# Optimization experiments

Measured on AMD Instinct MI355X. Metric: run time of the kernel, lower is better.

The kernel has to match this reference:

```python
import jax, jax.numpy as jnp
import numpy as np

B, L1, L2, D = 64, 512, 512, 256
NEG_INF = -1e10


def _leaky(x):
    return jax.nn.leaky_relu(x, negative_slope=0.01)


def setup_inputs() -> dict:
    key = jax.random.key(0)
    ks = jax.random.split(key, 12)
    s = 1.0 / np.sqrt(D)
    s2 = 1.0 / np.sqrt(2 * D)
    return {
        "r1": jax.random.normal(ks[0], (B, L1, D), jnp.float32),
        "r2": jax.random.normal(ks[1], (B, L2, D), jnp.float32),
        "mask1": jax.random.randint(ks[2], (B, L1, 1), 0, 2, jnp.int32),
        "mask2": jax.random.randint(ks[3], (B, L2, 1), 0, 2, jnp.int32),
        # mlp params (shared for r1 and r2, as in the torch module)
        "W1": jax.random.uniform(ks[4], (D, D), jnp.float32, -s, s),
        "b1": jnp.zeros((D,), jnp.float32),
        "W2": jax.random.uniform(ks[5], (D, D), jnp.float32, -s, s),
        "b2": jnp.zeros((D,), jnp.float32),
        # compare params
        "Wc1": jax.random.uniform(ks[6], (2 * D, D), jnp.float32, -s2, s2),
        "bc1": jnp.zeros((D,), jnp.float32),
        "Wc2": jax.random.uniform(ks[7], (D, D), jnp.float32, -s, s),
        "bc2": jnp.zeros((D,), jnp.float32),
    }


def _mlp(x, W1, b1, W2, b2):
    return _leaky(_leaky(x @ W1 + b1) @ W2 + b2)


def _compare(x, Wc1, bc1, Wc2, bc2):
    return _leaky(_leaky(x @ Wc1 + bc1) @ Wc2 + bc2)


def reference(r1, r2, mask1, mask2, W1, b1, W2, b2, Wc1, bc1, Wc2, bc2):
    # dropout layers are identity in eval mode
    m1 = mask1.astype(jnp.float32)  # [B,L1,1]
    m2 = mask2.astype(jnp.float32)  # [B,L2,1]

    h1 = _mlp(r1, W1, b1, W2, b2) * m1  # [B,L1,D]
    h2 = _mlp(r2, W1, b1, W2, b2) * m2  # [B,L2,D]

    lens1 = m1.sum(axis=1)  # [B,1]
    lens2 = m2.sum(axis=1)  # [B,1]

    # pairwise validity: matmul of expanded masks is D * outer(m1, m2);
    # only the sign is used downstream.
    pair = m1[:, :, 0][:, :, None] * m2[:, :, 0][:, None, :]  # [B,L1,L2]
    valid = pair > 0
    mask_inf = jnp.where(valid, 0.0, NEG_INF)

    o = jnp.einsum('bld,bmd->blm', h1, h2) + mask_inf  # [B,L1,L2]
    vf = valid.astype(o.dtype)
    o1 = jax.nn.softmax(o, axis=2) * vf
    o2 = jax.nn.softmax(o, axis=1) * vf

    r1_c = jnp.einsum('blm,bmd->bld', o1, h2)  # [B,L1,D]
    r2_c = jnp.einsum('blm,bld->bmd', o2, h1)  # [B,L2,D]

    r1_cmp = _compare(jnp.concatenate([h1, r1_c], axis=-1), Wc1, bc1, Wc2, bc2)
    r2_cmp = _compare(jnp.concatenate([h2, r2_c], axis=-1), Wc1, bc1, Wc2, bc2)

    r1_pool = (r1_cmp * m1).sum(axis=1) / lens1  # [B,D]
    r2_pool = (r2_cmp * m2).sum(axis=1) / lens2  # [B,D]
    return (r1_pool, r2_pool)
```

## Files before the change

### kernel.cpp

```cpp
#include <hip/hip_runtime.h>
#include <math.h>


using frag  = __attribute__((ext_vector_type(8))) short;
using f32x4 = __attribute__((ext_vector_type(4))) float;

constexpr int  LDK = 40;
constexpr int  KS  = 32;
constexpr long E   = 16777216L;

__device__ __forceinline__ float leaky(float x){ return x > 0.f ? x : 0.01f * x; }

__device__ __forceinline__ unsigned bf16_rne(float f){
    unsigned x = __float_as_uint(f);
    return (x + 0x7fffu + ((x >> 16) & 1u)) >> 16;
}
__device__ __forceinline__ unsigned pack_pair(float v){
    unsigned hi = bf16_rne(v);
    float fhi = __uint_as_float(hi << 16);
    unsigned lo = bf16_rne(v - fhi);
    return (hi << 16) | lo;
}

template<int AMODE, int BMODE, int EPI, int DUALA>
__global__ __launch_bounds__(512, 4)
void gemm_k(const unsigned* __restrict__ pa, const unsigned* __restrict__ pa2,
            const unsigned* __restrict__ pb, const float* __restrict__ bias,
            unsigned* __restrict__ pc,
            const int* __restrict__ mk1, const int* __restrict__ mk2,
            int M, int N, int K, int K1,
            int lda, int ldb, int ldc,
            long sA, long sB, long sC)
{
    __shared__ short As_hi[128 * LDK], As_lo[128 * LDK];
    __shared__ short Bs_hi[128 * LDK], Bs_lo[128 * LDK];

    const int z = blockIdx.z;
    const long aoff = (long)z * sA, boff = (long)z * sB, coff = (long)z * sC;
    const int m0 = blockIdx.x * 128, n0 = blockIdx.y * 128;
    const int tid  = threadIdx.x;
    const int lane = tid & 63;
    const int w    = tid >> 6;
    const int wr = w >> 2, wc = w & 3;
    const int lrow = lane & 15, lk = (lane >> 4) * 8;

    f32x4 acc[4][2];
#pragma unroll
    for (int i = 0; i < 4; ++i)
#pragma unroll
        for (int j = 0; j < 2; ++j) acc[i][j] = (f32x4){0.f, 0.f, 0.f, 0.f};

    for (int k0 = 0; k0 < K; k0 += KS) {
        if (AMODE == 0) {
            const int row = tid >> 2, k8 = (tid & 3) * 8;
            const unsigned* base = pa + aoff;
            int kk = k0;
            if (DUALA) { if (k0 >= K1) { base = pa2; kk = k0 - K1; } }
            const unsigned* src = base + (long)(m0 + row) * lda + kk + k8;
            uint4 wa = *(const uint4*)src;
            uint4 wb = *(const uint4*)(src + 4);
            uint4 hs, ls;
            hs.x = __builtin_amdgcn_perm(wa.y, wa.x, 0x07060302u);
            ls.x = __builtin_amdgcn_perm(wa.y, wa.x, 0x05040100u);
            hs.y = __builtin_amdgcn_perm(wa.w, wa.z, 0x07060302u);
            ls.y = __builtin_amdgcn_perm(wa.w, wa.z, 0x05040100u);
            hs.z = __builtin_amdgcn_perm(wb.y, wb.x, 0x07060302u);
            ls.z = __builtin_amdgcn_perm(wb.y, wb.x, 0x05040100u);
            hs.w = __builtin_amdgcn_perm(wb.w, wb.z, 0x07060302u);
            ls.w = __builtin_amdgcn_perm(wb.w, wb.z, 0x05040100u);
            *(uint4*)&As_hi[row * LDK + k8] = hs;
            *(uint4*)&As_lo[row * LDK + k8] = ls;
        } else if (AMODE == 1) {
            const int row = tid >> 2, k8 = (tid & 3) * 8;
            const int gr = m0 + row;
            const float* fb_ = (gr < 32768) ? ((const float*)pa  + (long)gr * lda)
                                            : ((const float*)pa2 + (long)(gr - 32768) * lda);
            const float* src = fb_ + k0 + k8;
            float4 fa = *(const float4*)src, fbv = *(const float4*)(src + 4);
            float f[8] = {fa.x, fa.y, fa.z, fa.w, fbv.x, fbv.y, fbv.z, fbv.w};
            unsigned hi[8], lo[8];
#pragma unroll
            for (int j = 0; j < 8; ++j) {
                hi[j] = bf16_rne(f[j]);
                lo[j] = bf16_rne(f[j] - __uint_as_float(hi[j] << 16));
            }
            uint4 hs = {hi[0] | (hi[1] << 16), hi[2] | (hi[3] << 16), hi[4] | (hi[5] << 16), hi[6] | (hi[7] << 16)};
            uint4 ls = {lo[0] | (lo[1] << 16), lo[2] | (lo[3] << 16), lo[4] | (lo[5] << 16), lo[6] | (lo[7] << 16)};
            *(uint4*)&As_hi[row * LDK + k8] = hs;
            *(uint4*)&As_lo[row * LDK + k8] = ls;
        } else {
            if (tid < 256) {
                const int k2 = ((tid >> 4) & 15) * 2, m8 = (tid & 15) * 8;
                const unsigned* s0 = pa + aoff + (long)(k0 + k2) * lda + m0 + m8;
                const unsigned* s1 = s0 + lda;
                uint4 a0 = *(const uint4*)s0, a1 = *(const uint4*)(s0 + 4);
                uint4 b0 = *(const uint4*)s1, b1 = *(const uint4*)(s1 + 4);
                unsigned wk[8]  = {a0.x, a0.y, a0.z, a0.w, a1.x, a1.y, a1.z, a1.w};
                unsigned wk1[8] = {b0.x, b0.y, b0.z, b0.w, b1.x, b1.y, b1.z, b1.w};
#pragma unroll
                for (int i = 0; i < 8; ++i) {
                    unsigned hw = __builtin_amdgcn_perm(wk1[i], wk[i], 0x07060302u);
                    unsigned lw = __builtin_amdgcn_perm(wk1[i], wk[i], 0x05040100u);
                    *(unsigned*)&As_hi[(m8 + i) * LDK + k2] = hw;
                    *(unsigned*)&As_lo[(m8 + i) * LDK + k2] = lw;
                }
            }
        }
        if (BMODE == 1) {
            const int row = tid >> 2, k8 = (tid & 3) * 8;
            const unsigned* src = pb + boff + (long)(n0 + row) * ldb + k0 + k8;
            uint4 wa = *(const uint4*)src;
            uint4 wb = *(const uint4*)(src + 4);
            uint4 hs, ls;
            hs.x = __builtin_amdgcn_perm(wa.y, wa.x, 0x07060302u);
            ls.x = __builtin_amdgcn_perm(wa.y, wa.x, 0x05040100u);
            hs.y = __builtin_amdgcn_perm(wa.w, wa.z, 0x07060302u);
            ls.y = __builtin_amdgcn_perm(wa.w, wa.z, 0x05040100u);
            hs.z = __builtin_amdgcn_perm(wb.y, wb.x, 0x07060302u);
            ls.z = __builtin_amdgcn_perm(wb.y, wb.x, 0x05040100u);
            hs.w = __builtin_amdgcn_perm(wb.w, wb.z, 0x07060302u);
            ls.w = __builtin_amdgcn_perm(wb.w, wb.z, 0x05040100u);
            *(uint4*)&Bs_hi[row * LDK + k8] = hs;
            *(uint4*)&Bs_lo[row * LDK + k8] = ls;
        } else if (BMODE == 0) {
            if (tid < 256) {
                const int k2 = ((tid >> 4) & 15) * 2, n8 = (tid & 15) * 8;
                const float* s0 = (const float*)pb + boff + (long)(k0 + k2) * ldb + n0 + n8;
                const float* s1 = s0 + ldb;
                float4 a0 = *(const float4*)s0, a1 = *(const float4*)(s0 + 4);
                float4 b0 = *(const float4*)s1, b1 = *(const float4*)(s1 + 4);
                float f0[8] = {a0.x, a0.y, a0.z, a0.w, a1.x, a1.y, a1.z, a1.w};
                float f1[8] = {b0.x, b0.y, b0.z, b0.w, b1.x, b1.y, b1.z, b1.w};
#pragma unroll
                for (int i = 0; i < 8; ++i) {
                    unsigned h0 = bf16_rne(f0[i]);
                    unsigned l0 = bf16_rne(f0[i] - __uint_as_float(h0 << 16));
                    unsigned h1 = bf16_rne(f1[i]);
                    unsigned l1 = bf16_rne(f1[i] - __uint_as_float(h1 << 16));
                    *(unsigned*)&Bs_hi[(n8 + i) * LDK + k2] = h0 | (h1 << 16);
                    *(unsigned*)&Bs_lo[(n8 + i) * LDK + k2] = l0 | (l1 << 16);
                }
            }
        } else {
            if (tid < 256) {
                const int k2 = ((tid >> 4) & 15) * 2, n8 = (tid & 15) * 8;
                const unsigned* s0 = pb + boff + (long)(k0 + k2) * ldb + n0 + n8;
                const unsigned* s1 = s0 + ldb;
                uint4 a0 = *(const uint4*)s0, a1 = *(const uint4*)(s0 + 4);
                uint4 b0 = *(const uint4*)s1, b1 = *(const uint4*)(s1 + 4);
                unsigned wk[8]  = {a0.x, a0.y, a0.z, a0.w, a1.x, a1.y, a1.z, a1.w};
                unsigned wk1[8] = {b0.x, b0.y, b0.z, b0.w, b1.x, b1.y, b1.z, b1.w};
#pragma unroll
                for (int i = 0; i < 8; ++i) {
                    unsigned hw = __builtin_amdgcn_perm(wk1[i], wk[i], 0x07060302u);
                    unsigned lw = __builtin_amdgcn_perm(wk1[i], wk[i], 0x05040100u);
                    *(unsigned*)&Bs_hi[(n8 + i) * LDK + k2] = hw;
                    *(unsigned*)&Bs_lo[(n8 + i) * LDK + k2] = lw;
                }
            }
        }
        __syncthreads();

        frag ah[4], al[4], bh[2], bl[2];
#pragma unroll
        for (int mi = 0; mi < 4; ++mi) {
            const int r = (wr * 64 + mi * 16 + lrow) * LDK + lk;
            ah[mi] = *(const frag*)&As_hi[r];
            al[mi] = *(const frag*)&As_lo[r];
        }
#pragma unroll
        for (int ni = 0; ni < 2; ++ni) {
            const int r = (wc * 32 + ni * 16 + lrow) * LDK + lk;
            bh[ni] = *(const frag*)&Bs_hi[r];
            bl[ni] = *(const frag*)&Bs_lo[r];
        }
#pragma unroll
        for (int mi = 0; mi < 4; ++mi)
#pragma unroll
            for (int ni = 0; ni < 2; ++ni) {
                acc[mi][ni] = __builtin_amdgcn_mfma_f32_16x16x32_bf16(ah[mi], bh[ni], acc[mi][ni], 0, 0, 0);
                acc[mi][ni] = __builtin_amdgcn_mfma_f32_16x16x32_bf16(ah[mi], bl[ni], acc[mi][ni], 0, 0, 0);
                acc[mi][ni] = __builtin_amdgcn_mfma_f32_16x16x32_bf16(al[mi], bh[ni], acc[mi][ni], 0, 0, 0);
            }
        __syncthreads();
    }

    float bvv[2];
    if (EPI == 2 || EPI == 3 || EPI == 4) {
#pragma unroll
        for (int ni = 0; ni < 2; ++ni) bvv[ni] = bias[n0 + wc * 32 + ni * 16 + lrow];
    }
#pragma unroll
    for (int mi = 0; mi < 4; ++mi)
#pragma unroll
        for (int ni = 0; ni < 2; ++ni) {
            const int col = n0 + wc * 32 + ni * 16 + lrow;
#pragma unroll
            for (int r = 0; r < 4; ++r) {
                const int row = m0 + wr * 64 + mi * 16 + (lane >> 4) * 4 + r;
                float v = acc[mi][ni][r];
                if (EPI == 2 || EPI == 3 || EPI == 4) v = leaky(v + bvv[ni]);
                if (EPI == 3) v *= (float)(row < 32768 ? mk1[row] : mk2[row - 32768]);
                const long off = coff + (long)row * ldc + col;
                if (EPI == 0 || EPI == 4) ((float*)pc)[off] = v;
                else                      pc[off] = pack_pair(v);
            }
        }
}

__global__ __launch_bounds__(256)
void softmax_row_k(const unsigned* __restrict__ S, const int* __restrict__ m1,
                   const int* __restrict__ m2, unsigned* __restrict__ O)
{
    const int tid = threadIdx.x;
    const int wid = tid >> 6, lane = tid & 63;
    const int gr = blockIdx.x * 4 + wid;
    const int b = gr >> 9, l = gr & 511;
    const unsigned* srow = S + (long)gr * 512;
    unsigned* orow = O + (long)gr * 512;
    const int rowvalid = m1[(long)b * 512 + l];
    const int* m2b = m2 + (long)b * 512;
    const int c8 = lane * 8;
    int4 ma = *(const int4*)(m2b + c8);
    int4 mb_ = *(const int4*)(m2b + c8 + 4);
    uint4 va = *(const uint4*)(srow + c8);
    uint4 vb = *(const uint4*)(srow + c8 + 4);
    float v[8] = {__uint_as_float(va.x), __uint_as_float(va.y), __uint_as_float(va.z), __uint_as_float(va.w),
                  __uint_as_float(vb.x), __uint_as_float(vb.y), __uint_as_float(vb.z), __uint_as_float(vb.w)};
    int mk[8] = {ma.x, ma.y, ma.z, ma.w, mb_.x, mb_.y, mb_.z, mb_.w};
    float mx = -3e38f;
#pragma unroll
    for (int j = 0; j < 8; ++j) if (mk[j]) mx = fmaxf(mx, v[j]);
#pragma unroll
    for (int o = 32; o; o >>= 1) mx = fmaxf(mx, __shfl_xor(mx, o));
    if (!rowvalid || mx < -1e30f) {
        uint4 zz = {0u, 0u, 0u, 0u};
        *(uint4*)(orow + c8) = zz; *(uint4*)(orow + c8 + 4) = zz;
        return;
    }
    float e[8]; float s = 0.f;
#pragma unroll
    for (int j = 0; j < 8; ++j) { e[j] = mk[j] ? __expf(v[j] - mx) : 0.f; s += e[j]; }
#pragma unroll
    for (int o = 32; o; o >>= 1) s += __shfl_xor(s, o);
    const float inv = 1.f / s;
    uint4 oa, ob;
    oa.x = pack_pair(e[0] * inv); oa.y = pack_pair(e[1] * inv);
    oa.z = pack_pair(e[2] * inv); oa.w = pack_pair(e[3] * inv);
    ob.x = pack_pair(e[4] * inv); ob.y = pack_pair(e[5] * inv);
    ob.z = pack_pair(e[6] * inv); ob.w = pack_pair(e[7] * inv);
    *(uint4*)(orow + c8) = oa;
    *(uint4*)(orow + c8 + 4) = ob;
}

__global__ __launch_bounds__(1024)
void softmax_col_k(const unsigned* __restrict__ S, const int* __restrict__ m1,
                   const int* __restrict__ m2, unsigned* __restrict__ O)
{
    __shared__ float red[16][64];
    __shared__ int m1s[512];
    const int b = blockIdx.y;
    const int c0 = blockIdx.x * 64;
    const int tid = threadIdx.x;
    const int c = tid & 63, rq = tid >> 6;
    if (tid < 512) m1s[tid] = m1[(long)b * 512 + tid];
    const int ac = m2[(long)b * 512 + c0 + c];
    const unsigned* Sb = S + (long)b * 512 * 512 + c0 + c;
    unsigned* Ob = O + (long)b * 512 * 512 + c0 + c;
    __syncthreads();

    float v[32];
#pragma unroll
    for (int g = 0; g < 32; ++g) {
        const int r = g * 16 + rq;
        float val = __uint_as_float(Sb[(long)r * 512]);
        v[g] = m1s[r] ? val : -3e38f;
    }
    float mx = -3e38f;
#pragma unroll
    for (int g = 0; g < 32; ++g) mx = fmaxf(mx, v[g]);
    red[rq][c] = mx;
    __syncthreads();
    float M = -3e38f;
#pragma unroll
    for (int i = 0; i < 16; ++i) M = fmaxf(M, red[i][c]);
    __syncthreads();
    float s = 0.f;
#pragma unroll
    for (int g = 0; g < 32; ++g) {
        float e = (v[g] > -1e30f) ? __expf(v[g] - M) : 0.f;
        v[g] = e;
        s += e;
    }
    red[rq][c] = s;
    __syncthreads();
    s = 0.f;
#pragma unroll
    for (int i = 0; i < 16; ++i) s += red[i][c];
    const float inv = (ac && s > 0.f) ? 1.f / s : 0.f;
#pragma unroll
    for (int g = 0; g < 32; ++g) {
        const int r = g * 16 + rq;
        Ob[(long)r * 512] = pack_pair(v[g] * inv);
    }
}

__global__ __launch_bounds__(256)
void pool_part_k(const float* __restrict__ RC, const int* __restrict__ m1,
                 const int* __restrict__ m2, float* __restrict__ part)
{
    const int rs = blockIdx.x, b = blockIdx.y, seg = blockIdx.z;
    const int* mb = (seg ? m2 : m1) + (long)b * 512;
    const float* base = RC + ((long)seg * 32768 + (long)b * 512) * 256;
    const int n = threadIdx.x;
    float acc = 0.f;
    for (int l = rs * 64; l < rs * 64 + 64; ++l)
        if (mb[l]) acc += base[(long)l * 256 + n];
    part[(((long)seg * 64 + b) * 8 + rs) * 256 + n] = acc;
}

__global__ __launch_bounds__(256)
void pool_red_k(const float* __restrict__ part, const int* __restrict__ m1,
                const int* __restrict__ m2, float* __restrict__ out)
{
    __shared__ float cr[256];
    const int g = blockIdx.x;
    const int seg = g >> 6, b = g & 63;
    const int n = threadIdx.x;
    const int* mb = (seg ? m2 : m1) + (long)b * 512;
    float s = 0.f;
#pragma unroll
    for (int i = 0; i < 8; ++i) s += part[((long)g * 8 + i) * 256 + n];
    float cpart = (float)(mb[n] + mb[n + 256]);
    cr[n] = cpart;
    __syncthreads();
    for (int o = 128; o; o >>= 1) { if (n < o) cr[n] += cr[n + o]; __syncthreads(); }
    out[(long)g * 256 + n] = s / cr[0];
}

extern "C" void kernel_launch(void* const* d_in, const int* in_sizes, int n_in,
                              void* d_out, int out_size, void* d_ws, size_t ws_size,
                              hipStream_t stream)
{
    const float* r1  = (const float*)d_in[0];
    const float* r2  = (const float*)d_in[1];
    const int*   mk1 = (const int*)d_in[2];
    const int*   mk2 = (const int*)d_in[3];
    const float* W1  = (const float*)d_in[4];
    const float* b1  = (const float*)d_in[5];
    const float* W2  = (const float*)d_in[6];
    const float* b2  = (const float*)d_in[7];
    const float* Wc1 = (const float*)d_in[8];
    const float* bc1 = (const float*)d_in[9];
    const float* Wc2 = (const float*)d_in[10];
    const float* bc2 = (const float*)d_in[11];
    float* out = (float*)d_out;

    unsigned* S0 = (unsigned*)d_ws;
    unsigned* S1 = S0 + E;
    unsigned* S2 = S0 + 2 * E;
    unsigned* S3 = S0 + 3 * E;
    const long H2OFF = 32768L * 256;

    dim3 blk(512), sblk(256);

    gemm_k<1,0,2,0><<<dim3(512,2,1), blk, 0, stream>>>(
        (const unsigned*)r1, (const unsigned*)r2, (const unsigned*)W1, b1, S1,
        nullptr, nullptr, 65536,256,256,0, 256,256,256, 0,0,0);
    gemm_k<0,0,3,0><<<dim3(512,2,1), blk, 0, stream>>>(
        S1, nullptr, (const unsigned*)W2, b2, S2,
        mk1, mk2, 65536,256,256,0, 256,256,256, 0,0,0);
    gemm_k<0,1,0,0><<<dim3(4,4,64), blk, 0, stream>>>(
        S2, nullptr, S2 + H2OFF, nullptr, S0,
        nullptr, nullptr, 512,512,256,0, 256,256,512, 131072,131072,262144);
    softmax_col_k<<<dim3(8,64), dim3(1024), 0, stream>>>(S0, mk1, mk2, S1);
    softmax_row_k<<<8192, sblk, 0, stream>>>(S0, mk1, mk2, S0);
    gemm_k<0,2,1,0><<<dim3(4,2,64), blk, 0, stream>>>(
        S0, nullptr, S2 + H2OFF, nullptr, S3,
        nullptr, nullptr, 512,256,512,0, 512,256,256, 262144,131072,131072);
    gemm_k<2,2,1,0><<<dim3(4,2,64), blk, 0, stream>>>(
        S1, nullptr, S2, nullptr, S3 + H2OFF,
        nullptr, nullptr, 512,256,512,0, 512,256,256, 262144,131072,131072);
    gemm_k<0,0,2,1><<<dim3(512,2,1), blk, 0, stream>>>(
        S2, S3, (const unsigned*)Wc1, bc1, S0,
        nullptr, nullptr, 65536,256,512,256, 256,256,256, 0,0,0);
    gemm_k<0,0,4,0><<<dim3(512,2,1), blk, 0, stream>>>(
        S0, nullptr, (const unsigned*)Wc2, bc2, S1,
        nullptr, nullptr, 65536,256,256,0, 256,256,256, 0,0,0);
    pool_part_k<<<dim3(8,64,2), sblk, 0, stream>>>((const float*)S1, mk1, mk2, (float*)S2);
    pool_red_k<<<128, sblk, 0, stream>>>((const float*)S2, mk1, mk2, out);
}
```

Before: 633.3 us.

## Store split-bf16 operands as separate hi/lo planes and load via global_load_lds

Intermediate tensors move from packed hi|lo 32-bit words to two separate bf16 planes, and weights are pre-transposed and split by a small conversion kernel. This lets the GEMM load A/B tiles directly into LDS with global_load_lds in fragment-ordered layout, removing the per-element perm unpacking and the padded LDS layout. The softmax outputs are written as transposed planes, so the column-softmax result feeds the GEMM the same way as the row one. The cost is extra conversion launches, strided 2-byte scalar loads for the transposed B path, and scattered short stores in the epilogues.

```diff
diff --git a/kernel.cpp b/kernel.cpp
--- a/kernel.cpp
+++ b/kernel.cpp
@@ -5,9 +5,7 @@
 using frag  = __attribute__((ext_vector_type(8))) short;
 using f32x4 = __attribute__((ext_vector_type(4))) float;
 
-constexpr int  LDK = 40;
-constexpr int  KS  = 32;
-constexpr long E   = 16777216L;
+constexpr long E = 16777216L;
 
 __device__ __forceinline__ float leaky(float x){ return x > 0.f ? x : 0.01f * x; }
 
@@ -15,34 +13,27 @@
     unsigned x = __float_as_uint(f);
     return (x + 0x7fffu + ((x >> 16) & 1u)) >> 16;
 }
-__device__ __forceinline__ unsigned pack_pair(float v){
-    unsigned hi = bf16_rne(v);
-    float fhi = __uint_as_float(hi << 16);
-    unsigned lo = bf16_rne(v - fhi);
-    return (hi << 16) | lo;
+
+__device__ __forceinline__ void gload16(const void* g, void* l){
+    __builtin_amdgcn_global_load_lds((const __attribute__((address_space(1))) void*)g,
+                                     (__attribute__((address_space(3))) void*)l, 16, 0, 0);
 }
 
 template<int AMODE, int BMODE, int EPI, int DUALA>
 __global__ __launch_bounds__(512, 4)
-void gemm_k(const unsigned* __restrict__ pa, const unsigned* __restrict__ pa2,
-            const unsigned* __restrict__ pb, const float* __restrict__ bias,
-            unsigned* __restrict__ pc,
+void gemm_k(const short* __restrict__ pa, const short* __restrict__ pa2,
+            const short* __restrict__ pb, const float* __restrict__ bias,
+            short* __restrict__ pc,
             const int* __restrict__ mk1, const int* __restrict__ mk2,
-            int M, int N, int K, int K1,
-            int lda, int ldb, int ldc,
-            long sA, long sB, long sC)
-{
-    __shared__ short As_hi[128 * LDK], As_lo[128 * LDK];
-    __shared__ short Bs_hi[128 * LDK], Bs_lo[128 * LDK];
-
+            int K, int K1, int lda, int ldb, int ldc,
+            long sA, long sB, long sC, long PSA, long PSB, long PSC)
+{
+    __shared__ __align__(16) short Ah[4096], Al[4096], Bh[4096], Bl[4096];
     const int z = blockIdx.z;
+    const int m0 = blockIdx.x * 128, n0 = blockIdx.y * 128;
+    const int tid = threadIdx.x, lane = tid & 63, w = tid >> 6;
+    const int wr = w >> 2, wc = w & 3;
     const long aoff = (long)z * sA, boff = (long)z * sB, coff = (long)z * sC;
-    const int m0 = blockIdx.x * 128, n0 = blockIdx.y * 128;
-    const int tid  = threadIdx.x;
-    const int lane = tid & 63;
-    const int w    = tid >> 6;
-    const int wr = w >> 2, wc = w & 3;
-    const int lrow = lane & 15, lk = (lane >> 4) * 8;
 
     f32x4 acc[4][2];
 #pragma unroll
@@ -50,137 +41,72 @@
 #pragma unroll
         for (int j = 0; j < 2; ++j) acc[i][j] = (f32x4){0.f, 0.f, 0.f, 0.f};
 
-    for (int k0 = 0; k0 < K; k0 += KS) {
+    for (int k0 = 0; k0 < K; k0 += 32) {
         if (AMODE == 0) {
-            const int row = tid >> 2, k8 = (tid & 3) * 8;
-            const unsigned* base = pa + aoff;
-            int kk = k0;
-            if (DUALA) { if (k0 >= K1) { base = pa2; kk = k0 - K1; } }
-            const unsigned* src = base + (long)(m0 + row) * lda + kk + k8;
-            uint4 wa = *(const uint4*)src;
-            uint4 wb = *(const uint4*)(src + 4);
-            uint4 hs, ls;
-            hs.x = __builtin_amdgcn_perm(wa.y, wa.x, 0x07060302u);
-            ls.x = __builtin_amdgcn_perm(wa.y, wa.x, 0x05040100u);
-            hs.y = __builtin_amdgcn_perm(wa.w, wa.z, 0x07060302u);
-            ls.y = __builtin_amdgcn_perm(wa.w, wa.z, 0x05040100u);
-            hs.z = __builtin_amdgcn_perm(wb.y, wb.x, 0x07060302u);
-            ls.z = __builtin_amdgcn_perm(wb.y, wb.x, 0x05040100u);
-            hs.w = __builtin_amdgcn_perm(wb.w, wb.z, 0x07060302u);
-            ls.w = __builtin_amdgcn_perm(wb.w, wb.z, 0x05040100u);
-            *(uint4*)&As_hi[row * LDK + k8] = hs;
-            *(uint4*)&As_lo[row * LDK + k8] = ls;
-        } else if (AMODE == 1) {
-            const int row = tid >> 2, k8 = (tid & 3) * 8;
-            const int gr = m0 + row;
-            const float* fb_ = (gr < 32768) ? ((const float*)pa  + (long)gr * lda)
-                                            : ((const float*)pa2 + (long)(gr - 32768) * lda);
-            const float* src = fb_ + k0 + k8;
-            float4 fa = *(const float4*)src, fbv = *(const float4*)(src + 4);
-            float f[8] = {fa.x, fa.y, fa.z, fa.w, fbv.x, fbv.y, fbv.z, fbv.w};
-            unsigned hi[8], lo[8];
+            const short* base = pa + aoff; int kk = k0;
+            if (DUALA) { if (k0 >= K1) { base = pa2 + aoff; kk = k0 - K1; } }
+            const short* s = base + (long)(m0 + w * 16 + (lane & 15)) * lda + kk + (lane >> 4) * 8;
+            gload16(s,       &Ah[w * 512]);
+            gload16(s + PSA, &Al[w * 512]);
+        } else {
+            const int gr = m0 + w * 16 + (lane & 15);
+            const float* f = (gr < 32768 ? (const float*)pa + (long)gr * lda
+                                         : (const float*)pa2 + (long)(gr - 32768) * lda)
+                             + k0 + (lane >> 4) * 8;
+            float4 u = *(const float4*)f, v4 = *(const float4*)(f + 4);
+            float fv[8] = {u.x, u.y, u.z, u.w, v4.x, v4.y, v4.z, v4.w};
+            unsigned hu[8], lu[8];
 #pragma unroll
             for (int j = 0; j < 8; ++j) {
-                hi[j] = bf16_rne(f[j]);
-                lo[j] = bf16_rne(f[j] - __uint_as_float(hi[j] << 16));
+                hu[j] = bf16_rne(fv[j]);
+                lu[j] = bf16_rne(fv[j] - __uint_as_float(hu[j] << 16));
             }
-            uint4 hs = {hi[0] | (hi[1] << 16), hi[2] | (hi[3] << 16), hi[4] | (hi[5] << 16), hi[6] | (hi[7] << 16)};
-            uint4 ls = {lo[0] | (lo[1] << 16), lo[2] | (lo[3] << 16), lo[4] | (lo[5] << 16), lo[6] | (lo[7] << 16)};
-            *(uint4*)&As_hi[row * LDK + k8] = hs;
-            *(uint4*)&As_lo[row * LDK + k8] = ls;
+            uint4 hs = {hu[0] | (hu[1] << 16), hu[2] | (hu[3] << 16), hu[4] | (hu[5] << 16), hu[6] | (hu[7] << 16)};
+            uint4 ls = {lu[0] | (lu[1] << 16), lu[2] | (lu[3] << 16), lu[4] | (lu[5] << 16), lu[6] | (lu[7] << 16)};
+            *(uint4*)&Ah[w * 512 + lane * 8] = hs;
+            *(uint4*)&Al[w * 512 + lane * 8] = ls;
+        }
+        if (BMODE == 0) {
+            const short* s = pb + boff + (long)(n0 + w * 16 + (lane & 15)) * ldb + k0 + (lane >> 4) * 8;
+            gload16(s,       &Bh[w * 512]);
+            gload16(s + PSB, &Bl[w * 512]);
         } else {
-            if (tid < 256) {
-                const int k2 = ((tid >> 4) & 15) * 2, m8 = (tid & 15) * 8;
-                const unsigned* s0 = pa + aoff + (long)(k0 + k2) * lda + m0 + m8;
-                const unsigned* s1 = s0 + lda;
-                uint4 a0 = *(const uint4*)s0, a1 = *(const uint4*)(s0 + 4);
-                uint4 b0 = *(const uint4*)s1, b1 = *(const uint4*)(s1 + 4);
-                unsigned wk[8]  = {a0.x, a0.y, a0.z, a0.w, a1.x, a1.y, a1.z, a1.w};
-                unsigned wk1[8] = {b0.x, b0.y, b0.z, b0.w, b1.x, b1.y, b1.z, b1.w};
-#pragma unroll
-                for (int i = 0; i < 8; ++i) {
-                    unsigned hw = __builtin_amdgcn_perm(wk1[i], wk[i], 0x07060302u);
-                    unsigned lw = __builtin_amdgcn_perm(wk1[i], wk[i], 0x05040100u);
-                    *(unsigned*)&As_hi[(m8 + i) * LDK + k2] = hw;
-                    *(unsigned*)&As_lo[(m8 + i) * LDK + k2] = lw;
-                }
+            const int kg = tid >> 7, nn = tid & 127;
+            const short* s = pb + boff + (long)(k0 + kg * 8) * ldb + n0 + nn;
+            unsigned hh[8], ll[8];
+#pragma unroll
+            for (int i = 0; i < 8; ++i) {
+                hh[i] = (unsigned short)s[(long)i * ldb];
+                ll[i] = (unsigned short)s[(long)i * ldb + PSB];
             }
-        }
-        if (BMODE == 1) {
-            const int row = tid >> 2, k8 = (tid & 3) * 8;
-            const unsigned* src = pb + boff + (long)(n0 + row) * ldb + k0 + k8;
-            uint4 wa = *(const uint4*)src;
-            uint4 wb = *(const uint4*)(src + 4);
-            uint4 hs, ls;
-            hs.x = __builtin_amdgcn_perm(wa.y, wa.x, 0x07060302u);
-            ls.x = __builtin_amdgcn_perm(wa.y, wa.x, 0x05040100u);
-            hs.y = __builtin_amdgcn_perm(wa.w, wa.z, 0x07060302u);
-            ls.y = __builtin_amdgcn_perm(wa.w, wa.z, 0x05040100u);
-            hs.z = __builtin_amdgcn_perm(wb.y, wb.x, 0x07060302u);
-            ls.z = __builtin_amdgcn_perm(wb.y, wb.x, 0x05040100u);
-            hs.w = __builtin_amdgcn_perm(wb.w, wb.z, 0x07060302u);
-            ls.w = __builtin_amdgcn_perm(wb.w, wb.z, 0x05040100u);
-            *(uint4*)&Bs_hi[row * LDK + k8] = hs;
-            *(uint4*)&Bs_lo[row * LDK + k8] = ls;
-        } else if (BMODE == 0) {
-            if (tid < 256) {
-                const int k2 = ((tid >> 4) & 15) * 2, n8 = (tid & 15) * 8;
-                const float* s0 = (const float*)pb + boff + (long)(k0 + k2) * ldb + n0 + n8;
-                const float* s1 = s0 + ldb;
-                float4 a0 = *(const float4*)s0, a1 = *(const float4*)(s0 + 4);
-                float4 b0 = *(const float4*)s1, b1 = *(const float4*)(s1 + 4);
-                float f0[8] = {a0.x, a0.y, a0.z, a0.w, a1.x, a1.y, a1.z, a1.w};
-                float f1[8] = {b0.x, b0.y, b0.z, b0.w, b1.x, b1.y, b1.z, b1.w};
-#pragma unroll
-                for (int i = 0; i < 8; ++i) {
-                    unsigned h0 = bf16_rne(f0[i]);
-                    unsigned l0 = bf16_rne(f0[i] - __uint_as_float(h0 << 16));
-                    unsigned h1 = bf16_rne(f1[i]);
-                    unsigned l1 = bf16_rne(f1[i] - __uint_as_float(h1 << 16));
-                    *(unsigned*)&Bs_hi[(n8 + i) * LDK + k2] = h0 | (h1 << 16);
-                    *(unsigned*)&Bs_lo[(n8 + i) * LDK + k2] = l0 | (l1 << 16);
-                }
-            }
-        } else {
-            if (tid < 256) {
-                const int k2 = ((tid >> 4) & 15) * 2, n8 = (tid & 15) * 8;
-                const unsigned* s0 = pb + boff + (long)(k0 + k2) * ldb + n0 + n8;
-                const unsigned* s1 = s0 + ldb;
-                uint4 a0 = *(const uint4*)s0, a1 = *(const uint4*)(s0 + 4);
-                uint4 b0 = *(const uint4*)s1, b1 = *(const uint4*)(s1 + 4);
-                unsigned wk[8]  = {a0.x, a0.y, a0.z, a0.w, a1.x, a1.y, a1.z, a1.w};
-                unsigned wk1[8] = {b0.x, b0.y, b0.z, b0.w, b1.x, b1.y, b1.z, b1.w};
-#pragma unroll
-                for (int i = 0; i < 8; ++i) {
-                    unsigned hw = __builtin_amdgcn_perm(wk1[i], wk[i], 0x07060302u);
-                    unsigned lw = __builtin_amdgcn_perm(wk1[i], wk[i], 0x05040100u);
-                    *(unsigned*)&Bs_hi[(n8 + i) * LDK + k2] = hw;
-                    *(unsigned*)&Bs_lo[(n8 + i) * LDK + k2] = lw;
-                }
-            }
+            uint4 hw = {hh[0] | (hh[1] << 16), hh[2] | (hh[3] << 16), hh[4] | (hh[5] << 16), hh[6] | (hh[7] << 16)};
+            uint4 lw = {ll[0] | (ll[1] << 16), ll[2] | (ll[3] << 16), ll[4] | (ll[5] << 16), ll[6] | (ll[7] << 16)};
+            const int d = (nn >> 4) * 512 + (kg * 16 + (nn & 15)) * 8;
+            *(uint4*)&Bh[d] = hw;
+            *(uint4*)&Bl[d] = lw;
         }
         __syncthreads();
 
-        frag ah[4], al[4], bh[2], bl[2];
+        frag fah[4], fal[4], fbh[2], fbl[2];
 #pragma unroll
         for (int mi = 0; mi < 4; ++mi) {
-            const int r = (wr * 64 + mi * 16 + lrow) * LDK + lk;
-            ah[mi] = *(const frag*)&As_hi[r];
-            al[mi] = *(const frag*)&As_lo[r];
+            const int off = (wr * 4 + mi) * 512 + lane * 8;
+            fah[mi] = *(const frag*)&Ah[off];
+            fal[mi] = *(const frag*)&Al[off];
         }
 #pragma unroll
         for (int ni = 0; ni < 2; ++ni) {
-            const int r = (wc * 32 + ni * 16 + lrow) * LDK + lk;
-            bh[ni] = *(const frag*)&Bs_hi[r];
-            bl[ni] = *(const frag*)&Bs_lo[r];
+            const int off = (wc * 2 + ni) * 512 + lane * 8;
+            fbh[ni] = *(const frag*)&Bh[off];
+            fbl[ni] = *(const frag*)&Bl[off];
         }
 #pragma unroll
         for (int mi = 0; mi < 4; ++mi)
 #pragma unroll
             for (int ni = 0; ni < 2; ++ni) {
-                acc[mi][ni] = __builtin_amdgcn_mfma_f32_16x16x32_bf16(ah[mi], bh[ni], acc[mi][ni], 0, 0, 0);
-                acc[mi][ni] = __builtin_amdgcn_mfma_f32_16x16x32_bf16(ah[mi], bl[ni], acc[mi][ni], 0, 0, 0);
-                acc[mi][ni] = __builtin_amdgcn_mfma_f32_16x16x32_bf16(al[mi], bh[ni], acc[mi][ni], 0, 0, 0);
+                acc[mi][ni] = __builtin_amdgcn_mfma_f32_16x16x32_bf16(fah[mi], fbh[ni], acc[mi][ni], 0, 0, 0);
+                acc[mi][ni] = __builtin_amdgcn_mfma_f32_16x16x32_bf16(fah[mi], fbl[ni], acc[mi][ni], 0, 0, 0);
+                acc[mi][ni] = __builtin_amdgcn_mfma_f32_16x16x32_bf16(fal[mi], fbh[ni], acc[mi][ni], 0, 0, 0);
             }
         __syncthreads();
     }
@@ -188,13 +114,13 @@
     float bvv[2];
     if (EPI == 2 || EPI == 3 || EPI == 4) {
 #pragma unroll
-        for (int ni = 0; ni < 2; ++ni) bvv[ni] = bias[n0 + wc * 32 + ni * 16 + lrow];
+        for (int ni = 0; ni < 2; ++ni) bvv[ni] = bias[n0 + wc * 32 + ni * 16 + (lane & 15)];
     }
 #pragma unroll
     for (int mi = 0; mi < 4; ++mi)
 #pragma unroll
         for (int ni = 0; ni < 2; ++ni) {
-            const int col = n0 + wc * 32 + ni * 16 + lrow;
+            const int col = n0 + wc * 32 + ni * 16 + (lane & 15);
 #pragma unroll
             for (int r = 0; r < 4; ++r) {
                 const int row = m0 + wr * 64 + mi * 16 + (lane >> 4) * 4 + r;
@@ -202,31 +128,46 @@
                 if (EPI == 2 || EPI == 3 || EPI == 4) v = leaky(v + bvv[ni]);
                 if (EPI == 3) v *= (float)(row < 32768 ? mk1[row] : mk2[row - 32768]);
                 const long off = coff + (long)row * ldc + col;
-                if (EPI == 0 || EPI == 4) ((float*)pc)[off] = v;
-                else                      pc[off] = pack_pair(v);
+                if (EPI == 0 || EPI == 4) {
+                    ((float*)pc)[off] = v;
+                } else {
+                    unsigned hu = bf16_rne(v);
+                    pc[off]       = (short)hu;
+                    pc[off + PSC] = (short)bf16_rne(v - __uint_as_float(hu << 16));
+                }
             }
         }
 }
 
 __global__ __launch_bounds__(256)
-void softmax_row_k(const unsigned* __restrict__ S, const int* __restrict__ m1,
-                   const int* __restrict__ m2, unsigned* __restrict__ O)
+void wconv_k(const float* __restrict__ W, short* __restrict__ T, int Kd, long PS)
+{
+    const int idx = blockIdx.x * 256 + threadIdx.x;
+    const int n = idx & 255, k = idx >> 8;
+    const float v = W[idx];
+    const unsigned hu = bf16_rne(v);
+    T[(long)n * Kd + k]      = (short)hu;
+    T[(long)n * Kd + k + PS] = (short)bf16_rne(v - __uint_as_float(hu << 16));
+}
+
+__global__ __launch_bounds__(256)
+void softmax_row_k(const float* __restrict__ S, const int* __restrict__ m1,
+                   const int* __restrict__ m2, short* __restrict__ O)
 {
     const int tid = threadIdx.x;
     const int wid = tid >> 6, lane = tid & 63;
     const int gr = blockIdx.x * 4 + wid;
     const int b = gr >> 9, l = gr & 511;
-    const unsigned* srow = S + (long)gr * 512;
-    unsigned* orow = O + (long)gr * 512;
+    const float* srow = S + (long)gr * 512;
+    short* orow = O + (long)gr * 512;
     const int rowvalid = m1[(long)b * 512 + l];
     const int* m2b = m2 + (long)b * 512;
     const int c8 = lane * 8;
     int4 ma = *(const int4*)(m2b + c8);
     int4 mb_ = *(const int4*)(m2b + c8 + 4);
-    uint4 va = *(const uint4*)(srow + c8);
-    uint4 vb = *(const uint4*)(srow + c8 + 4);
-    float v[8] = {__uint_as_float(va.x), __uint_as_float(va.y), __uint_as_float(va.z), __uint_as_float(va.w),
-                  __uint_as_float(vb.x), __uint_as_float(vb.y), __uint_as_float(vb.z), __uint_as_float(vb.w)};
+    float4 va = *(const float4*)(srow + c8);
+    float4 vb = *(const float4*)(srow + c8 + 4);
+    float v[8] = {va.x, va.y, va.z, va.w, vb.x, vb.y, vb.z, vb.w};
     int mk[8] = {ma.x, ma.y, ma.z, ma.w, mb_.x, mb_.y, mb_.z, mb_.w};
     float mx = -3e38f;
 #pragma unroll
@@ -235,7 +176,8 @@
     for (int o = 32; o; o >>= 1) mx = fmaxf(mx, __shfl_xor(mx, o));
     if (!rowvalid || mx < -1e30f) {
         uint4 zz = {0u, 0u, 0u, 0u};
-        *(uint4*)(orow + c8) = zz; *(uint4*)(orow + c8 + 4) = zz;
+        *(uint4*)&orow[c8] = zz;
+        *(uint4*)&orow[c8 + E] = zz;
         return;
     }
     float e[8]; float s = 0.f;
@@ -244,18 +186,25 @@
 #pragma unroll
     for (int o = 32; o; o >>= 1) s += __shfl_xor(s, o);
     const float inv = 1.f / s;
-    uint4 oa, ob;
-    oa.x = pack_pair(e[0] * inv); oa.y = pack_pair(e[1] * inv);
-    oa.z = pack_pair(e[2] * inv); oa.w = pack_pair(e[3] * inv);
-    ob.x = pack_pair(e[4] * inv); ob.y = pack_pair(e[5] * inv);
-    ob.z = pack_pair(e[6] * inv); ob.w = pack_pair(e[7] * inv);
-    *(uint4*)(orow + c8) = oa;
-    *(uint4*)(orow + c8 + 4) = ob;
+    unsigned short oh[8], ol[8];
+#pragma unroll
+    for (int j = 0; j < 8; ++j) {
+        float p = e[j] * inv;
+        unsigned hu = bf16_rne(p);
+        oh[j] = (unsigned short)hu;
+        ol[j] = (unsigned short)bf16_rne(p - __uint_as_float(hu << 16));
+    }
+    uint4 hs = {oh[0] | ((unsigned)oh[1] << 16), oh[2] | ((unsigned)oh[3] << 16),
+                oh[4] | ((unsigned)oh[5] << 16), oh[6] | ((unsigned)oh[7] << 16)};
+    uint4 ls = {ol[0] | ((unsigned)ol[1] << 16), ol[2] | ((unsigned)ol[3] << 16),
+                ol[4] | ((unsigned)ol[5] << 16), ol[6] | ((unsigned)ol[7] << 16)};
+    *(uint4*)&orow[c8] = hs;
+    *(uint4*)&orow[c8 + E] = ls;
 }
 
 __global__ __launch_bounds__(1024)
-void softmax_col_k(const unsigned* __restrict__ S, const int* __restrict__ m1,
-                   const int* __restrict__ m2, unsigned* __restrict__ O)
+void softmax_col_k(const float* __restrict__ S, const int* __restrict__ m1,
+                   const int* __restrict__ m2, short* __restrict__ O)
 {
     __shared__ float red[16][64];
     __shared__ int m1s[512];
@@ -265,15 +214,14 @@
     const int c = tid & 63, rq = tid >> 6;
     if (tid < 512) m1s[tid] = m1[(long)b * 512 + tid];
     const int ac = m2[(long)b * 512 + c0 + c];
-    const unsigned* Sb = S + (long)b * 512 * 512 + c0 + c;
-    unsigned* Ob = O + (long)b * 512 * 512 + c0 + c;
+    const float* Sb = S + (long)b * 262144 + c0 + c;
     __syncthreads();
 
     float v[32];
 #pragma unroll
     for (int g = 0; g < 32; ++g) {
         const int r = g * 16 + rq;
-        float val = __uint_as_float(Sb[(long)r * 512]);
+        float val = Sb[(long)r * 512];
         v[g] = m1s[r] ? val : -3e38f;
     }
     float mx = -3e38f;
@@ -298,10 +246,14 @@
 #pragma unroll
     for (int i = 0; i < 16; ++i) s += red[i][c];
     const float inv = (ac && s > 0.f) ? 1.f / s : 0.f;
+    short* oc = O + (long)b * 262144 + (long)(c0 + c) * 512;
 #pragma unroll
     for (int g = 0; g < 32; ++g) {
         const int r = g * 16 + rq;
-        Ob[(long)r * 512] = pack_pair(v[g] * inv);
+        float p = v[g] * inv;
+        unsigned hu = bf16_rne(p);
+        oc[r]     = (short)hu;
+        oc[r + E] = (short)bf16_rne(p - __uint_as_float(hu << 16));
     }
 }
 
@@ -331,8 +283,7 @@
     float s = 0.f;
 #pragma unroll
     for (int i = 0; i < 8; ++i) s += part[((long)g * 8 + i) * 256 + n];
-    float cpart = (float)(mb[n] + mb[n + 256]);
-    cr[n] = cpart;
+    cr[n] = (float)(mb[n] + mb[n + 256]);
     __syncthreads();
     for (int o = 128; o; o >>= 1) { if (n < o) cr[n] += cr[n + o]; __syncthreads(); }
     out[(long)g * 256 + n] = s / cr[0];
@@ -356,37 +307,43 @@
     const float* bc2 = (const float*)d_in[11];
     float* out = (float*)d_out;
 
-    unsigned* S0 = (unsigned*)d_ws;
-    unsigned* S1 = S0 + E;
-    unsigned* S2 = S0 + 2 * E;
-    unsigned* S3 = S0 + 3 * E;
-    const long H2OFF = 32768L * 256;
-
-    dim3 blk(512), sblk(256);
-
-    gemm_k<1,0,2,0><<<dim3(512,2,1), blk, 0, stream>>>(
-        (const unsigned*)r1, (const unsigned*)r2, (const unsigned*)W1, b1, S1,
-        nullptr, nullptr, 65536,256,256,0, 256,256,256, 0,0,0);
-    gemm_k<0,0,3,0><<<dim3(512,2,1), blk, 0, stream>>>(
-        S1, nullptr, (const unsigned*)W2, b2, S2,
-        mk1, mk2, 65536,256,256,0, 256,256,256, 0,0,0);
-    gemm_k<0,1,0,0><<<dim3(4,4,64), blk, 0, stream>>>(
-        S2, nullptr, S2 + H2OFF, nullptr, S0,
-        nullptr, nullptr, 512,512,256,0, 256,256,512, 131072,131072,262144);
-    softmax_col_k<<<dim3(8,64), dim3(1024), 0, stream>>>(S0, mk1, mk2, S1);
-    softmax_row_k<<<8192, sblk, 0, stream>>>(S0, mk1, mk2, S0);
-    gemm_k<0,2,1,0><<<dim3(4,2,64), blk, 0, stream>>>(
-        S0, nullptr, S2 + H2OFF, nullptr, S3,
-        nullptr, nullptr, 512,256,512,0, 512,256,256, 262144,131072,131072);
-    gemm_k<2,2,1,0><<<dim3(4,2,64), blk, 0, stream>>>(
-        S1, nullptr, S2, nullptr, S3 + H2OFF,
-        nullptr, nullptr, 512,256,512,0, 512,256,256, 262144,131072,131072);
-    gemm_k<0,0,2,1><<<dim3(512,2,1), blk, 0, stream>>>(
-        S2, S3, (const unsigned*)Wc1, bc1, S0,
-        nullptr, nullptr, 65536,256,512,256, 256,256,256, 0,0,0);
-    gemm_k<0,0,4,0><<<dim3(512,2,1), blk, 0, stream>>>(
-        S0, nullptr, (const unsigned*)Wc2, bc2, S1,
-        nullptr, nullptr, 65536,256,256,0, 256,256,256, 0,0,0);
-    pool_part_k<<<dim3(8,64,2), sblk, 0, stream>>>((const float*)S1, mk1, mk2, (float*)S2);
-    pool_red_k<<<128, sblk, 0, stream>>>((const float*)S2, mk1, mk2, out);
-}
+    short* S0s = (short*)d_ws;
+    short* S1s = S0s + 2 * E;
+    short* S2s = S0s + 4 * E;
+    short* S3s = S0s + 6 * E;
+    short* Wt1  = S0s;
+    short* Wt2  = S0s + 131072;
+    short* WtC1 = S1s;
+    short* WtC2 = S1s + 262144;
+    const long H2 = 8388608;
+
+    wconv_k<<<256, 256, 0, stream>>>(W1, Wt1, 256, 65536);
+    wconv_k<<<256, 256, 0, stream>>>(W2, Wt2, 256, 65536);
+    gemm_k<1,0,2,0><<<dim3(512,2,1), 512, 0, stream>>>(
+        (const short*)r1, (const short*)r2, Wt1, b1, S1s, nullptr, nullptr,
+        256, 0, 256, 256, 256, 0, 0, 0, 0, 65536, E);
+    gemm_k<0,0,3,0><<<dim3(512,2,1), 512, 0, stream>>>(
+        S1s, nullptr, Wt2, b2, S2s, mk1, mk2,
+        256, 0, 256, 256, 256, 0, 0, 0, E, 65536, E);
+    gemm_k<0,0,0,0><<<dim3(4,4,64), 512, 0, stream>>>(
+        S2s, nullptr, S2s + H2, nullptr, S0s, nullptr, nullptr,
+        256, 0, 256, 256, 512, 131072, 131072, 262144, E, E, 0);
+    softmax_col_k<<<dim3(8,64), 1024, 0, stream>>>((const float*)S0s, mk1, mk2, S1s);
+    softmax_row_k<<<8192, 256, 0, stream>>>((const float*)S0s, mk1, mk2, S3s);
+    gemm_k<0,1,1,0><<<dim3(4,2,64), 512, 0, stream>>>(
+        S3s, nullptr, S2s + H2, nullptr, S0s, nullptr, nullptr,
+        512, 0, 512, 256, 256, 262144, 131072, 131072, E, E, E);
+    gemm_k<0,1,1,0><<<dim3(4,2,64), 512, 0, stream>>>(
+        S1s, nullptr, S2s, nullptr, S0s + H2, nullptr, nullptr,
+        512, 0, 512, 256, 256, 262144, 131072, 131072, E, E, E);
+    wconv_k<<<512, 256, 0, stream>>>(Wc1, WtC1, 512, 131072);
+    wconv_k<<<256, 256, 0, stream>>>(Wc2, WtC2, 256, 65536);
+    gemm_k<0,0,2,1><<<dim3(512,2,1), 512, 0, stream>>>(
+        S2s, S0s, WtC1, bc1, S3s, nullptr, nullptr,
+        512, 256, 256, 512, 256, 0, 0, 0, E, 131072, E);
+    gemm_k<0,0,4,0><<<dim3(512,2,1), 512, 0, stream>>>(
+        S3s, nullptr, WtC2, bc2, S2s, nullptr, nullptr,
+        256, 0, 256, 256, 256, 0, 0, 0, E, 65536, 0);
+    pool_part_k<<<dim3(8,64,2), 256, 0, stream>>>((const float*)S2s, mk1, mk2, (float*)S0s);
+    pool_red_k<<<128, 256, 0, stream>>>((const float*)S0s, mk1, mk2, out);
+}
```

New measurement: 682.2 us. 1.08x slower.
